# Kernel optimization log

Hardware: AMD Instinct MI355X
Metric: run time of the kernel (lower is better)

The kernel has to match this reference:

```python
import jax, jax.numpy as jnp
import numpy as np
import math

C_S, C_Z = 384, 128
N_HEAD, C = 12, 16
N_QP, N_PV = 4, 8
B, N_RES = 1, 384


def quat_to_rot(q):
    # q: (..., 4) unnormalized quaternion -> (..., 3, 3) rotation matrix
    q = q / jnp.linalg.norm(q, axis=-1, keepdims=True)
    w, x, y, z = q[..., 0], q[..., 1], q[..., 2], q[..., 3]
    R = jnp.stack([
        1 - 2 * (y * y + z * z), 2 * (x * y - w * z), 2 * (x * z + w * y),
        2 * (x * y + w * z), 1 - 2 * (x * x + z * z), 2 * (y * z - w * x),
        2 * (x * z - w * y), 2 * (y * z + w * x), 1 - 2 * (x * x + y * y),
    ], axis=-1)
    return R.reshape(q.shape[:-1] + (3, 3))


def warp_3d_point(T, p):
    # T: (..., 1, 1, N, 4, 4) rigid transforms; p: (..., H, P, N, 3)
    R = T[..., :3, :3]
    t = T[..., :3, 3]
    return jnp.squeeze(R @ p[..., None], -1) + t


def warp_3d_point_inv(T, p):
    # Inverse rigid transform: R^T (p - t)
    R = T[..., :3, :3]
    t = T[..., :3, 3]
    return jnp.squeeze(jnp.swapaxes(R, -1, -2) @ (p - t)[..., None], -1)


def setup_inputs() -> dict:
    key = jax.random.key(0)
    ks = jax.random.split(key, 24)
    s = jax.random.normal(ks[0], (B, N_RES, C_S), dtype=jnp.float32)
    z = jax.random.normal(ks[1], (B, N_RES, N_RES, C_Z), dtype=jnp.float32)
    # Build rigid backbone transforms T (rotation from random quaternion + translation)
    quat = jax.random.normal(ks[2], (B, N_RES, 4), dtype=jnp.float32)
    trans = jax.random.normal(ks[3], (B, N_RES, 3), dtype=jnp.float32) * 10.0
    R = quat_to_rot(quat)
    T = jnp.zeros((B, N_RES, 4, 4), dtype=jnp.float32)
    T = T.at[..., :3, :3].set(R)
    T = T.at[..., :3, 3].set(trans)
    T = T.at[..., 3, 3].set(1.0)

    def lin(k, din, dout):
        kw, kb = jax.random.split(k)
        W = jax.random.normal(kw, (din, dout), dtype=jnp.float32) * 0.02
        b = jax.random.normal(kb, (dout,), dtype=jnp.float32) * 0.01
        return W, b

    Wq, bq = lin(ks[4], C_S, N_HEAD * C)
    Wk, bk = lin(ks[5], C_S, N_HEAD * C)
    Wv, bv = lin(ks[6], C_S, N_HEAD * C)
    Wqp, bqp = lin(ks[7], C_S, 3 * N_QP * N_HEAD)
    Wkp, bkp = lin(ks[8], C_S, 3 * N_QP * N_HEAD)
    Wvp, bvp = lin(ks[9], C_S, 3 * N_PV * N_HEAD)
    Wb, bb = lin(ks[10], C_Z, N_HEAD)
    d_out_in = N_HEAD * C_Z + N_HEAD * C + N_HEAD * 4 * N_PV
    Wo, bo = lin(ks[11], d_out_in, C_S)
    head_weights = jax.random.normal(ks[12], (N_HEAD,), dtype=jnp.float32) * 0.1
    return dict(s=s, z=z, T=T, Wq=Wq, bq=bq, Wk=Wk, bk=bk, Wv=Wv, bv=bv,
                Wqp=Wqp, bqp=bqp, Wkp=Wkp, bkp=bkp, Wvp=Wvp, bvp=bvp,
                Wb=Wb, bb=bb, Wo=Wo, bo=bo, head_weights=head_weights)


def ipa_forward(s, z, T, Wq, bq, Wk, bk, Wv, bv, Wqp, bqp, Wkp, bkp,
                Wvp, bvp, Wb, bb, Wo, bo, head_weights):
    batch = s.shape[:-2]
    n = s.shape[-2]
    # --- prepare qkv ---
    def heads(x):  # (..., N, H*C) -> (..., H, N, C)
        return jnp.moveaxis(x.reshape(batch + (n, N_HEAD, C)), -3, -2)
    q = heads(s @ Wq + bq)
    k = heads(s @ Wk + bk)
    v = heads(s @ Wv + bv)

    def pts(x, P):  # (..., N, 3*H*P) -> (..., H, P, N, 3)
        x = x.reshape(batch + (n, 3, N_HEAD, P))
        return jnp.moveaxis(x, (-4, -3), (-2, -1))
    qp = pts(s @ Wqp + bqp, N_QP)
    kp = pts(s @ Wkp + bkp, N_QP)
    vp = pts(s @ Wvp + bvp, N_PV)

    # --- attention scores (Alg 22 line 7) ---
    wc = math.sqrt(2.0 / (9.0 * N_QP))
    wl = math.sqrt(1.0 / 3.0)
    gamma = jax.nn.softplus(head_weights).reshape(-1, 1, 1)  # (H,1,1)
    q = q * (1.0 / math.sqrt(C))
    bias = jnp.moveaxis(z @ Wb + bb, -1, -3)  # (..., H, N, N)
    qk = jnp.einsum('...hic,...hjc->...hij', q, k)
    T_bc = T.reshape(batch + (1, 1, n, 4, 4))
    tqp = warp_3d_point(T_bc, qp)[..., :, None, :]   # (..., H, QP, N, 1, 3)
    tkp = warp_3d_point(T_bc, kp)[..., None, :, :]   # (..., H, QP, 1, N, 3)
    sq_dist = jnp.sum((tqp - tkp) ** 2, axis=-1)      # (..., H, QP, N, N)
    qpkp_term = gamma * (wc / 2.0) * jnp.sum(sq_dist, axis=-3)  # (..., H, N, N)
    att = jax.nn.softmax(wl * (qk + bias - qpkp_term), axis=-1)

    # --- outputs ---
    pairwise = jnp.einsum('...ijc,...hij->...hic', z, att)
    pairwise = jnp.moveaxis(pairwise, -3, -2).reshape(batch + (n, N_HEAD * C_Z))
    v_out = jnp.einsum('...hij,...hjc->...hic', att, v)
    v_out = jnp.moveaxis(v_out, -3, -2).reshape(batch + (n, N_HEAD * C))
    vt = warp_3d_point(T_bc, vp)                                # (..., H, PV, N, 3)
    v_att = jnp.einsum('...hij,...hkjp->...hkip', att, vt)     # (..., H, PV, N, 3)
    v_tr = warp_3d_point_inv(T_bc, v_att)                       # (..., H, PV, N, 3)
    v_tr = jnp.einsum('...hpic->...ichp', v_tr)                 # (..., N, 3, H, PV)
    norm = jnp.linalg.norm(v_tr, axis=-3, keepdims=True)        # (..., N, 1, H, PV)
    vp_norm = norm.reshape(batch + (n, N_HEAD * N_PV))
    vp_out = v_tr.reshape(batch + (n, 3 * N_HEAD * N_PV))

    out = jnp.concatenate([v_out, vp_out, vp_norm, pairwise], axis=-1)
    return out @ Wo + bo


def reference(s, z, T, Wq, bq, Wk, bk, Wv, bv, Wqp, bqp, Wkp, bkp,
              Wvp, bvp, Wb, bb, Wo, bo, head_weights):
    return ipa_forward(s, z, T, Wq, bq, Wk, bk, Wv, bv, Wqp, bqp, Wkp, bkp,
                       Wvp, bvp, Wb, bb, Wo, bo, head_weights)
```

## Files before the change

kernel.cpp:

```cpp
#include <hip/hip_runtime.h>
#include <math.h>

#define NRES 384
#define NH   12
#define WLc 0.5773502691896258f
#define WCc 0.23570226039551587f

typedef __attribute__((ext_vector_type(8))) _Float16 half8;
typedef __attribute__((ext_vector_type(4))) float f32x4;

#define OFF_P    0
#define OFF_PW   0
#define OFF_SH   442368
#define OFF_WCT  516096
#define OFF_BCT  737280
#define OFF_QE   738432
#define OFF_KE   885888
#define OFF_VET  1033344
#define OFF_WOT  1143936
#define OFF_CAT  1549440
#define OFF_ATT  1660032
#define OFF_BIAS 2544768

__global__ __launch_bounds__(256) void pack_kernel(
    const float* __restrict__ s,
    const float* __restrict__ Wq,  const float* __restrict__ bq,
    const float* __restrict__ Wk,  const float* __restrict__ bk,
    const float* __restrict__ Wv,  const float* __restrict__ bv,
    const float* __restrict__ Wqp, const float* __restrict__ bqp,
    const float* __restrict__ Wkp, const float* __restrict__ bkp,
    const float* __restrict__ Wvp, const float* __restrict__ bvp,
    const float* __restrict__ Wo,  const float* __restrict__ bo,
    float* __restrict__ ws, float* __restrict__ out)
{
    int b = blockIdx.x, t = threadIdx.x;
    _Float16* sh  = (_Float16*)(ws + OFF_SH);
    _Float16* wct = (_Float16*)(ws + OFF_WCT);
    _Float16* wot = (_Float16*)(ws + OFF_WOT);
    float* bct = ws + OFF_BCT;

    if (b < 144) {
        int id = b * 256 + t;
        float4 v = ((const float4*)s)[id];
        _Float16 r[4] = { (_Float16)v.x, (_Float16)v.y, (_Float16)v.z, (_Float16)v.w };
        *(uint2*)(sh + id * 4) = *(uint2*)r;
        return;
    }
    __shared__ float tile[64 * 65];
    if (b < 252) {
        int ti = b - 144;
        int k0 = (ti % 6) * 64, n0 = (ti / 6) * 64;
        int cl = t & 63, rg = t >> 6;
        int ncat = n0 + cl;
        const float* W; int dout, col;
        if      (ncat < 192) { W = Wq;  dout = 192; col = ncat; }
        else if (ncat < 384) { W = Wk;  dout = 192; col = ncat - 192; }
        else if (ncat < 576) { W = Wv;  dout = 192; col = ncat - 384; }
        else if (ncat < 720) { W = Wqp; dout = 144; col = ncat - 576; }
        else if (ncat < 864) { W = Wkp; dout = 144; col = ncat - 720; }
        else                 { W = Wvp; dout = 288; col = ncat - 864; }
        #pragma unroll
        for (int u = 0; u < 16; u++) {
            int r = rg * 16 + u;
            tile[r * 65 + cl] = W[(size_t)(k0 + r) * dout + col];
        }
        __syncthreads();
        #pragma unroll
        for (int u2 = 0; u2 < 2; u2++) {
            int item = t + 256 * u2;
            int nl = item >> 3, kg = item & 7;
            half8 rr;
            #pragma unroll
            for (int jj = 0; jj < 8; jj++) rr[jj] = (_Float16)tile[(kg * 8 + jj) * 65 + nl];
            *(half8*)(wct + (size_t)(n0 + nl) * 384 + k0 + kg * 8) = rr;
        }
        return;
    }
    if (b < 450) {
        int ti = b - 252;
        int k0 = (ti % 33) * 64, n0 = (ti / 33) * 64;
        int cl = t & 63, rg = t >> 6;
        #pragma unroll
        for (int u = 0; u < 16; u++) {
            int r = rg * 16 + u;
            tile[r * 65 + cl] = Wo[(size_t)(k0 + r) * 384 + n0 + cl];
        }
        __syncthreads();
        #pragma unroll
        for (int u2 = 0; u2 < 2; u2++) {
            int item = t + 256 * u2;
            int nl = item >> 3, kg = item & 7;
            half8 rr;
            #pragma unroll
            for (int jj = 0; jj < 8; jj++) rr[jj] = (_Float16)tile[(kg * 8 + jj) * 65 + nl];
            *(half8*)(wot + (size_t)(n0 + nl) * 2112 + k0 + kg * 8) = rr;
        }
        return;
    }
    if (b == 450) {
        for (int e = t; e < 1152; e += 256) {
            float bv_;
            if      (e < 192) bv_ = bq[e];
            else if (e < 384) bv_ = bk[e - 192];
            else if (e < 576) bv_ = bv[e - 384];
            else if (e < 720) bv_ = bqp[e - 576];
            else if (e < 864) bv_ = bkp[e - 720];
            else              bv_ = bvp[e - 864];
            bct[e] = bv_;
        }
        return;
    }
    {
        int idx = (b - 451) * 256 + t;
        out[idx] = bo[idx % 384];
    }
}

__global__ __launch_bounds__(256) void proj_mfma(float* __restrict__ ws)
{
    const _Float16* sh  = (const _Float16*)(ws + OFF_SH);
    const _Float16* wct = (const _Float16*)(ws + OFF_WCT);
    const float* bct = ws + OFF_BCT;
    float* P = ws + OFF_P;

    int t = threadIdx.x, w = t >> 6, lane = t & 63;
    int m = lane & 15, q = lane >> 4;
    int n0 = blockIdx.x * 64, m0 = blockIdx.y * 64 + w * 16;

    f32x4 acc[4] = {0};
    const _Float16* arow = sh + (size_t)(m0 + m) * 384;
    #pragma unroll 4
    for (int s = 0; s < 12; s++) {
        int k = s * 32 + q * 8;
        half8 a = *(const half8*)(arow + k);
        #pragma unroll
        for (int nt = 0; nt < 4; nt++) {
            half8 b = *(const half8*)(wct + (size_t)(n0 + nt * 16 + m) * 384 + k);
            acc[nt] = __builtin_amdgcn_mfma_f32_16x16x32_f16(a, b, acc[nt], 0, 0, 0);
        }
    }
    #pragma unroll
    for (int nt = 0; nt < 4; nt++) {
        int col = n0 + nt * 16 + m;
        float bias = bct[col];
        #pragma unroll
        for (int r = 0; r < 4; r++)
            P[(size_t)(m0 + q * 4 + r) * 1152 + col] = acc[nt][r] + bias;
    }
}

__global__ __launch_bounds__(192) void prep_kernel(
    const float* __restrict__ T, const float* __restrict__ hw,
    float* __restrict__ ws)
{
    int i = blockIdx.x, t = threadIdx.x;
    const float* pr = ws + OFF_P + (size_t)i * 1152;
    float* Qe = ws + OFF_QE;
    float* Ke = ws + OFF_KE;
    _Float16* vet = (_Float16*)(ws + OFF_VET);

    __shared__ float sT[16], sG[12];
    __shared__ float sTQ[12][4][3], sTK[12][4][3];
    if (t < 16) sT[t] = T[i * 16 + t];
    if (t < 12) { float x = hw[t]; sG[t] = (x > 20.f) ? x : log1pf(__expf(x)); }
    __syncthreads();
    float R00=sT[0],R01=sT[1],R02=sT[2],t0=sT[3];
    float R10=sT[4],R11=sT[5],R12=sT[6],t1=sT[7];
    float R20=sT[8],R21=sT[9],R22=sT[10],t2=sT[11];

    if (t < 48) {
        int h = t >> 2, p = t & 3;
        float a0 = pr[576 + 0*48 + h*4 + p], a1 = pr[576 + 1*48 + h*4 + p], a2 = pr[576 + 2*48 + h*4 + p];
        sTQ[h][p][0] = R00*a0 + R01*a1 + R02*a2 + t0;
        sTQ[h][p][1] = R10*a0 + R11*a1 + R12*a2 + t1;
        sTQ[h][p][2] = R20*a0 + R21*a1 + R22*a2 + t2;
    } else if (t < 96) {
        int tt = t - 48, h = tt >> 2, p = tt & 3;
        float a0 = pr[720 + 0*48 + h*4 + p], a1 = pr[720 + 1*48 + h*4 + p], a2 = pr[720 + 2*48 + h*4 + p];
        sTK[h][p][0] = R00*a0 + R01*a1 + R02*a2 + t0;
        sTK[h][p][1] = R10*a0 + R11*a1 + R12*a2 + t1;
        sTK[h][p][2] = R20*a0 + R21*a1 + R22*a2 + t2;
    } else {
        int tt = t - 96, h = tt >> 3, p = tt & 7;
        float a0 = pr[864 + 0*96 + h*8 + p], a1 = pr[864 + 1*96 + h*8 + p], a2 = pr[864 + 2*96 + h*8 + p];
        vet[(size_t)(h*48 + 16 + p*3 + 0) * 384 + i] = (_Float16)(R00*a0 + R01*a1 + R02*a2 + t0);
        vet[(size_t)(h*48 + 16 + p*3 + 1) * 384 + i] = (_Float16)(R10*a0 + R11*a1 + R12*a2 + t1);
        vet[(size_t)(h*48 + 16 + p*3 + 2) * 384 + i] = (_Float16)(R20*a0 + R21*a1 + R22*a2 + t2);
    }
    {
        int h = t >> 4, c = t & 15;
        vet[(size_t)(h*48 + c) * 384 + i] = (_Float16)pr[384 + h*16 + c];
        if (t < 96) vet[(size_t)((t>>3)*48 + 40 + (t&7)) * 384 + i] = (_Float16)0.f;
        Qe[(size_t)i*384 + h*32 + c] = WLc * 0.25f * pr[h*16 + c];
        Ke[((size_t)h*384 + i)*32 + c] = pr[192 + h*16 + c];
    }
    __syncthreads();
    if (t < 144) {
        int h = t / 12, d = t % 12, p = d / 3, r = d % 3;
        float gw = WLc * sG[h] * WCc;
        Qe[(size_t)i*384 + h*32 + 16 + d] = gw * sTQ[h][p][r];
        Ke[((size_t)h*384 + i)*32 + 16 + d] = sTK[h][p][r];
    }
    if (t < 12) {
        int h = t;
        float sqq = 0.f, sqk = 0.f;
        #pragma unroll
        for (int p = 0; p < 4; p++)
            #pragma unroll
            for (int r = 0; r < 3; r++) { sqq += sTQ[h][p][r]*sTQ[h][p][r]; sqk += sTK[h][p][r]*sTK[h][p][r]; }
        float gw = WLc * sG[h] * WCc;
        Qe[(size_t)i*384 + h*32 + 28] = -0.5f * gw;
        Qe[(size_t)i*384 + h*32 + 29] = -0.5f * gw * sqq;
        Qe[(size_t)i*384 + h*32 + 30] = 0.f;
        Qe[(size_t)i*384 + h*32 + 31] = 0.f;
        Ke[((size_t)h*384 + i)*32 + 28] = sqk;
        Ke[((size_t)h*384 + i)*32 + 29] = 1.f;
        Ke[((size_t)h*384 + i)*32 + 30] = 0.f;
        Ke[((size_t)h*384 + i)*32 + 31] = 0.f;
    }
}

__global__ __launch_bounds__(256) void bias_mfma(
    const float* __restrict__ z, const float* __restrict__ Wb,
    const float* __restrict__ bb, float* __restrict__ ws)
{
    __shared__ _Float16 zb[64 * 136];
    __shared__ _Float16 wbT[16 * 136];
    __shared__ float sbb[16];
    _Float16* biasb = (_Float16*)(ws + OFF_BIAS);
    int b = blockIdx.x, t = threadIdx.x;

    if (b < 576) {
        ((float4*)(ws + OFF_PW))[b * 256 + t] = (float4){0.f, 0.f, 0.f, 0.f};
    }

    size_t m0 = (size_t)b * 64;
    {
        int r = t >> 2, co = (t & 3) * 32;
        const float* zr = z + (m0 + r) * 128 + co;
        #pragma unroll
        for (int u = 0; u < 4; u++) {
            float4 v0 = ((const float4*)zr)[u * 2 + 0];
            float4 v1 = ((const float4*)zr)[u * 2 + 1];
            half8 rr;
            rr[0]=(_Float16)v0.x; rr[1]=(_Float16)v0.y; rr[2]=(_Float16)v0.z; rr[3]=(_Float16)v0.w;
            rr[4]=(_Float16)v1.x; rr[5]=(_Float16)v1.y; rr[6]=(_Float16)v1.z; rr[7]=(_Float16)v1.w;
            *(half8*)(zb + r * 136 + co + u * 8) = rr;
        }
    }
    if (t < 128) {
        #pragma unroll
        for (int h = 0; h < 12; h++) wbT[h * 136 + t] = (_Float16)(WLc * Wb[t * 12 + h]);
        #pragma unroll
        for (int h = 12; h < 16; h++) wbT[h * 136 + t] = (_Float16)0.f;
    }
    if (t < 16) sbb[t] = (t < 12) ? WLc * bb[t] : 0.f;
    __syncthreads();

    int w = t >> 6, lane = t & 63;
    int m = lane & 15, q = lane >> 4;
    f32x4 acc = {0};
    #pragma unroll
    for (int s = 0; s < 4; s++) {
        int k = s * 32 + q * 8;
        half8 a = *(const half8*)(zb + (w * 16 + m) * 136 + k);
        half8 bfr = *(const half8*)(wbT + m * 136 + k);
        acc = __builtin_amdgcn_mfma_f32_16x16x32_f16(a, bfr, acc, 0, 0, 0);
    }
    if (m < 12) {
        #pragma unroll
        for (int r = 0; r < 4; r++) {
            size_t ri = m0 + w * 16 + q * 4 + r;
            biasb[(size_t)m * 147456 + ri] = (_Float16)(acc[r] + sbb[m]);
        }
    }
}

__global__ __launch_bounds__(512) void logits_kernel(float* __restrict__ ws)
{
    __shared__ float sQe[8 * 32];
    __shared__ float sLg[8][384];
    __shared__ float sMS[16];

    int h = blockIdx.y, i0 = blockIdx.x * 8;
    int t = threadIdx.x;
    const float* Qe = ws + OFF_QE;
    const float* Ke = ws + OFF_KE;
    const _Float16* biasb = (const _Float16*)(ws + OFF_BIAS);
    _Float16* attg = (_Float16*)(ws + OFF_ATT);

    if (t < 256)
        sQe[t] = Qe[(size_t)(i0 + (t >> 5)) * 384 + h * 32 + (t & 31)];
    __syncthreads();

    float lgv[8];
    if (t < 384) {
        int j = t;
        float ke[32];
        const float4* kr = (const float4*)(Ke + ((size_t)h * 384 + j) * 32);
        #pragma unroll
        for (int u = 0; u < 8; u++) { float4 v = kr[u]; ke[u*4]=v.x; ke[u*4+1]=v.y; ke[u*4+2]=v.z; ke[u*4+3]=v.w; }
        #pragma unroll
        for (int ii = 0; ii < 8; ii++) {
            float acc = (float)biasb[(size_t)h * 147456 + (size_t)(i0 + ii) * 384 + j];
            #pragma unroll
            for (int c = 0; c < 32; c++) acc += sQe[ii * 32 + c] * ke[c];
            lgv[ii] = acc;
            sLg[ii][j] = acc;
        }
    }
    __syncthreads();
    {
        int w = t >> 6, lane = t & 63;
        float vv[6], mx = -1e30f;
        #pragma unroll
        for (int u = 0; u < 6; u++) { vv[u] = sLg[w][lane + 64 * u]; mx = fmaxf(mx, vv[u]); }
        #pragma unroll
        for (int off = 1; off < 64; off <<= 1) mx = fmaxf(mx, __shfl_xor(mx, off));
        float sm = 0.f;
        #pragma unroll
        for (int u = 0; u < 6; u++) sm += __expf(vv[u] - mx);
        #pragma unroll
        for (int off = 1; off < 64; off <<= 1) sm += __shfl_xor(sm, off);
        if (lane == 0) { sMS[w] = mx; sMS[8 + w] = sm; }
    }
    __syncthreads();
    if (t < 384) {
        int j = t;
        #pragma unroll
        for (int ii = 0; ii < 8; ii++) {
            float a = __expf(lgv[ii] - sMS[ii]) * (1.0f / sMS[8 + ii]);
            attg[((size_t)h * 384 + i0 + ii) * 384 + j] = (_Float16)a;
        }
    }
}

__global__ __launch_bounds__(256) void pairwise_mfma(
    const float* __restrict__ z, float* __restrict__ ws)
{
    __shared__ _Float16 ztT[128 * 136];
    int i = blockIdx.x, jc = blockIdx.y, j0 = jc * 128;
    int t = threadIdx.x, w = t >> 6, lane = t & 63;
    int m16 = lane & 15, q = lane >> 4;
    const _Float16* attg = (const _Float16*)(ws + OFF_ATT);
    float* PW = ws + OFF_PW;

    {
        int c = t & 127, jg = t >> 7;
        const float* zbase = z + ((size_t)i * 384 + j0 + jg * 8) * 128 + c;
        #pragma unroll
        for (int jt = 0; jt < 8; jt++) {
            half8 r;
            #pragma unroll
            for (int u = 0; u < 8; u++)
                r[u] = (_Float16)zbase[(size_t)(jt * 16 + u) * 128];
            *(half8*)(ztT + c * 136 + jt * 16 + jg * 8) = r;
        }
    }
    __syncthreads();

    f32x4 acc0 = {0}, acc1 = {0};
    const _Float16* arow = attg + ((size_t)(m16 < 12 ? m16 : 0) * 384 + i) * 384 + j0;
    #pragma unroll
    for (int ks = 0; ks < 4; ks++) {
        int k = ks * 32 + q * 8;
        half8 a;
        if (m16 < 12) a = *(const half8*)(arow + k);
        else          a = (half8){0,0,0,0,0,0,0,0};
        half8 b0 = *(const half8*)(ztT + (w * 32 + m16) * 136 + k);
        half8 b1 = *(const half8*)(ztT + (w * 32 + 16 + m16) * 136 + k);
        acc0 = __builtin_amdgcn_mfma_f32_16x16x32_f16(a, b0, acc0, 0, 0, 0);
        acc1 = __builtin_amdgcn_mfma_f32_16x16x32_f16(a, b1, acc1, 0, 0, 0);
    }
    if (q < 3) {
        #pragma unroll
        for (int r = 0; r < 4; r++) {
            int h = q * 4 + r;
            atomicAdd(&PW[(size_t)i * 1536 + h * 128 + w * 32 + m16],      acc0[r]);
            atomicAdd(&PW[(size_t)i * 1536 + h * 128 + w * 32 + 16 + m16], acc1[r]);
        }
    }
}

__global__ __launch_bounds__(128) void out40_ep(
    const float* __restrict__ T, float* __restrict__ ws)
{
    const _Float16* attg = (const _Float16*)(ws + OFF_ATT);
    const _Float16* vet  = (const _Float16*)(ws + OFF_VET);
    _Float16* catb = (_Float16*)(ws + OFF_CAT);

    int h = blockIdx.y, t = threadIdx.x, w = t >> 6, lane = t & 63;
    int m16 = lane & 15, q = lane >> 4;
    int i0 = blockIdx.x * 32;

    __shared__ float sO[32 * 49];
    __shared__ float sTT[32 * 17];
    for (int e = t; e < 512; e += 128)
        sTT[(e >> 4) * 17 + (e & 15)] = T[(size_t)(i0 + (e >> 4)) * 16 + (e & 15)];

    f32x4 acc[3] = {0};
    const _Float16* arow = attg + ((size_t)h * 384 + i0 + w * 16 + m16) * 384;
    #pragma unroll 3
    for (int s = 0; s < 12; s++) {
        int k = s * 32 + q * 8;
        half8 a = *(const half8*)(arow + k);
        #pragma unroll
        for (int nt = 0; nt < 3; nt++) {
            half8 b = *(const half8*)(vet + (size_t)(h * 48 + nt * 16 + m16) * 384 + k);
            acc[nt] = __builtin_amdgcn_mfma_f32_16x16x32_f16(a, b, acc[nt], 0, 0, 0);
        }
    }
    #pragma unroll
    for (int nt = 0; nt < 3; nt++)
        #pragma unroll
        for (int r = 0; r < 4; r++)
            sO[(w * 16 + q * 4 + r) * 49 + nt * 16 + m16] = acc[nt][r];
    __syncthreads();

    for (int e = t; e < 512; e += 128) {
        int il = e >> 4, c = e & 15;
        catb[(size_t)(i0 + il) * 576 + h * 16 + c] = (_Float16)sO[il * 49 + c];
    }
    for (int e = t; e < 256; e += 128) {
        int il = e >> 3, p = e & 7;
        const float* o = sO + il * 49 + 16 + p * 3;
        const float* Ti = sTT + il * 17;
        float x0 = o[0] - Ti[3], x1 = o[1] - Ti[7], x2 = o[2] - Ti[11];
        float r0 = Ti[0]*x0 + Ti[4]*x1 + Ti[8]*x2;
        float r1 = Ti[1]*x0 + Ti[5]*x1 + Ti[9]*x2;
        float r2 = Ti[2]*x0 + Ti[6]*x1 + Ti[10]*x2;
        _Float16* cr = catb + (size_t)(i0 + il) * 576;
        cr[192 + 0*96 + h*8 + p] = (_Float16)r0;
        cr[192 + 1*96 + h*8 + p] = (_Float16)r1;
        cr[192 + 2*96 + h*8 + p] = (_Float16)r2;
        cr[480 + h*8 + p] = (_Float16)sqrtf(r0*r0 + r1*r1 + r2*r2);
    }
}

__global__ __launch_bounds__(128) void outgemm_mfma(float* __restrict__ ws, float* __restrict__ out)
{
    const _Float16* catb = (const _Float16*)(ws + OFF_CAT);
    const float* PW = ws + OFF_PW;
    const _Float16* wot = (const _Float16*)(ws + OFF_WOT);

    int t = threadIdx.x, w = t >> 6, lane = t & 63;
    int m = lane & 15, q = lane >> 4;
    int n0 = blockIdx.x * 64;
    int m0 = blockIdx.y * 32 + w * 16;
    int kbase = blockIdx.z * 352;

    f32x4 acc[4] = {0};
    int row = m0 + m;
    #pragma unroll 2
    for (int s = 0; s < 11; s++) {
        int kb = kbase + s * 32;
        int k = kb + q * 8;
        half8 a;
        if (kb < 576) {
            a = *(const half8*)(catb + (size_t)row * 576 + k);
        } else {
            const float* pwp = PW + (size_t)row * 1536 + (k - 576);
            float4 u0 = ((const float4*)pwp)[0];
            float4 u1 = ((const float4*)pwp)[1];
            a[0]=(_Float16)u0.x; a[1]=(_Float16)u0.y; a[2]=(_Float16)u0.z; a[3]=(_Float16)u0.w;
            a[4]=(_Float16)u1.x; a[5]=(_Float16)u1.y; a[6]=(_Float16)u1.z; a[7]=(_Float16)u1.w;
        }
        #pragma unroll
        for (int nt = 0; nt < 4; nt++) {
            half8 b = *(const half8*)(wot + (size_t)(n0 + nt * 16 + m) * 2112 + k);
            acc[nt] = __builtin_amdgcn_mfma_f32_16x16x32_f16(a, b, acc[nt], 0, 0, 0);
        }
    }
    #pragma unroll
    for (int nt = 0; nt < 4; nt++) {
        int col = n0 + nt * 16 + m;
        #pragma unroll
        for (int r = 0; r < 4; r++)
            atomicAdd(&out[(size_t)(m0 + q * 4 + r) * 384 + col], acc[nt][r]);
    }
}

extern "C" void kernel_launch(void* const* d_in, const int* in_sizes, int n_in,
                              void* d_out, int out_size, void* d_ws, size_t ws_size,
                              hipStream_t stream)
{
    const float* s   = (const float*)d_in[0];
    const float* z   = (const float*)d_in[1];
    const float* T   = (const float*)d_in[2];
    const float* Wq  = (const float*)d_in[3];
    const float* bq  = (const float*)d_in[4];
    const float* Wk  = (const float*)d_in[5];
    const float* bk  = (const float*)d_in[6];
    const float* Wv  = (const float*)d_in[7];
    const float* bv  = (const float*)d_in[8];
    const float* Wqp = (const float*)d_in[9];
    const float* bqp = (const float*)d_in[10];
    const float* Wkp = (const float*)d_in[11];
    const float* bkp = (const float*)d_in[12];
    const float* Wvp = (const float*)d_in[13];
    const float* bvp = (const float*)d_in[14];
    const float* Wb  = (const float*)d_in[15];
    const float* bb  = (const float*)d_in[16];
    const float* Wo  = (const float*)d_in[17];
    const float* bo  = (const float*)d_in[18];
    const float* hw  = (const float*)d_in[19];
    float* ws  = (float*)d_ws;
    float* out = (float*)d_out;

    pack_kernel<<<1027, 256, 0, stream>>>(s, Wq, bq, Wk, bk, Wv, bv,
                                          Wqp, bqp, Wkp, bkp, Wvp, bvp, Wo, bo, ws, out);
    proj_mfma<<<dim3(18, 6), 256, 0, stream>>>(ws);
    prep_kernel<<<384, 192, 0, stream>>>(T, hw, ws);
    bias_mfma<<<2304, 256, 0, stream>>>(z, Wb, bb, ws);
    logits_kernel<<<dim3(48, 12), 512, 0, stream>>>(ws);
    pairwise_mfma<<<dim3(384, 3), 256, 0, stream>>>(z, ws);
    out40_ep<<<dim3(12, 12), 128, 0, stream>>>(T, ws);
    outgemm_mfma<<<dim3(6, 12, 6), 128, 0, stream>>>(ws, out);
}
```

Baseline: 212.0 us.

## Fuse bias GEMM into pack kernel and attention-value epilogue into logits kernel

Merges the z-bias MFMA into the packing launch and reads z straight from global memory into MFMA fragments, skipping the LDS staging. Folds the attention-times-value and inverse-rigid epilogue into the logits kernel, using the softmax output already held in shared memory, and moves the out-bias init and PW zeroing there as well. Halves the proj_mfma block size to put more blocks on the grid. The goal is fewer launches and no reread of the attention matrix. In exchange the logits kernel uses more LDS and runs a half-empty MFMA (only 8 of 16 rows valid), and the merged pack kernel has heterogeneous blocks.

```diff
diff --git a/kernel.cpp b/kernel.cpp
--- a/kernel.cpp
+++ b/kernel.cpp
@@ -22,18 +22,58 @@
 #define OFF_ATT  1660032
 #define OFF_BIAS 2544768
 
-__global__ __launch_bounds__(256) void pack_kernel(
-    const float* __restrict__ s,
+__global__ __launch_bounds__(256) void pack_bias(
+    const float* __restrict__ s,  const float* __restrict__ z,
     const float* __restrict__ Wq,  const float* __restrict__ bq,
     const float* __restrict__ Wk,  const float* __restrict__ bk,
     const float* __restrict__ Wv,  const float* __restrict__ bv,
     const float* __restrict__ Wqp, const float* __restrict__ bqp,
     const float* __restrict__ Wkp, const float* __restrict__ bkp,
     const float* __restrict__ Wvp, const float* __restrict__ bvp,
-    const float* __restrict__ Wo,  const float* __restrict__ bo,
-    float* __restrict__ ws, float* __restrict__ out)
+    const float* __restrict__ Wb,  const float* __restrict__ bb,
+    const float* __restrict__ Wo,
+    float* __restrict__ ws)
 {
     int b = blockIdx.x, t = threadIdx.x;
+    __shared__ float tile[64 * 65];
+    __shared__ _Float16 wbT[16 * 136];
+    __shared__ float sbb[16];
+
+    if (b >= 451) {
+        _Float16* biasb = (_Float16*)(ws + OFF_BIAS);
+        int bi = b - 451;
+        size_t m0 = (size_t)bi * 64;
+        if (t < 128) {
+            #pragma unroll
+            for (int h = 0; h < 12; h++) wbT[h * 136 + t] = (_Float16)(WLc * Wb[t * 12 + h]);
+            #pragma unroll
+            for (int h = 12; h < 16; h++) wbT[h * 136 + t] = (_Float16)0.f;
+        }
+        if (t < 16) sbb[t] = (t < 12) ? WLc * bb[t] : 0.f;
+        __syncthreads();
+        int w = t >> 6, lane = t & 63;
+        int m = lane & 15, q = lane >> 4;
+        size_t ri = m0 + w * 16 + m;
+        const float* zr = z + ri * 128 + q * 8;
+        f32x4 acc = {0};
+        #pragma unroll
+        for (int sI = 0; sI < 4; sI++) {
+            float4 v0 = *(const float4*)(zr + sI * 32);
+            float4 v1 = *(const float4*)(zr + sI * 32 + 4);
+            half8 a;
+            a[0]=(_Float16)v0.x; a[1]=(_Float16)v0.y; a[2]=(_Float16)v0.z; a[3]=(_Float16)v0.w;
+            a[4]=(_Float16)v1.x; a[5]=(_Float16)v1.y; a[6]=(_Float16)v1.z; a[7]=(_Float16)v1.w;
+            half8 bf = *(const half8*)(wbT + m * 136 + sI * 32 + q * 8);
+            acc = __builtin_amdgcn_mfma_f32_16x16x32_f16(a, bf, acc, 0, 0, 0);
+        }
+        if (m < 12) {
+            #pragma unroll
+            for (int r = 0; r < 4; r++)
+                biasb[(size_t)m * 147456 + m0 + w * 16 + q * 4 + r] = (_Float16)(acc[r] + sbb[m]);
+        }
+        return;
+    }
+
     _Float16* sh  = (_Float16*)(ws + OFF_SH);
     _Float16* wct = (_Float16*)(ws + OFF_WCT);
     _Float16* wot = (_Float16*)(ws + OFF_WOT);
@@ -46,7 +86,6 @@
         *(uint2*)(sh + id * 4) = *(uint2*)r;
         return;
     }
-    __shared__ float tile[64 * 65];
     if (b < 252) {
         int ti = b - 144;
         int k0 = (ti % 6) * 64, n0 = (ti / 6) * 64;
@@ -97,26 +136,19 @@
         }
         return;
     }
-    if (b == 450) {
-        for (int e = t; e < 1152; e += 256) {
-            float bv_;
-            if      (e < 192) bv_ = bq[e];
-            else if (e < 384) bv_ = bk[e - 192];
-            else if (e < 576) bv_ = bv[e - 384];
-            else if (e < 720) bv_ = bqp[e - 576];
-            else if (e < 864) bv_ = bkp[e - 720];
-            else              bv_ = bvp[e - 864];
-            bct[e] = bv_;
-        }
-        return;
-    }
-    {
-        int idx = (b - 451) * 256 + t;
-        out[idx] = bo[idx % 384];
-    }
-}
-
-__global__ __launch_bounds__(256) void proj_mfma(float* __restrict__ ws)
+    for (int e = t; e < 1152; e += 256) {
+        float bv_;
+        if      (e < 192) bv_ = bq[e];
+        else if (e < 384) bv_ = bk[e - 192];
+        else if (e < 576) bv_ = bv[e - 384];
+        else if (e < 720) bv_ = bqp[e - 576];
+        else if (e < 864) bv_ = bkp[e - 720];
+        else              bv_ = bvp[e - 864];
+        bct[e] = bv_;
+    }
+}
+
+__global__ __launch_bounds__(128) void proj_mfma(float* __restrict__ ws)
 {
     const _Float16* sh  = (const _Float16*)(ws + OFF_SH);
     const _Float16* wct = (const _Float16*)(ws + OFF_WCT);
@@ -125,7 +157,7 @@
 
     int t = threadIdx.x, w = t >> 6, lane = t & 63;
     int m = lane & 15, q = lane >> 4;
-    int n0 = blockIdx.x * 64, m0 = blockIdx.y * 64 + w * 16;
+    int n0 = blockIdx.x * 64, m0 = blockIdx.y * 32 + w * 16;
 
     f32x4 acc[4] = {0};
     const _Float16* arow = sh + (size_t)(m0 + m) * 384;
@@ -220,77 +252,38 @@
     }
 }
 
-__global__ __launch_bounds__(256) void bias_mfma(
-    const float* __restrict__ z, const float* __restrict__ Wb,
-    const float* __restrict__ bb, float* __restrict__ ws)
-{
-    __shared__ _Float16 zb[64 * 136];
-    __shared__ _Float16 wbT[16 * 136];
-    __shared__ float sbb[16];
-    _Float16* biasb = (_Float16*)(ws + OFF_BIAS);
-    int b = blockIdx.x, t = threadIdx.x;
-
-    if (b < 576) {
-        ((float4*)(ws + OFF_PW))[b * 256 + t] = (float4){0.f, 0.f, 0.f, 0.f};
-    }
-
-    size_t m0 = (size_t)b * 64;
-    {
-        int r = t >> 2, co = (t & 3) * 32;
-        const float* zr = z + (m0 + r) * 128 + co;
-        #pragma unroll
-        for (int u = 0; u < 4; u++) {
-            float4 v0 = ((const float4*)zr)[u * 2 + 0];
-            float4 v1 = ((const float4*)zr)[u * 2 + 1];
-            half8 rr;
-            rr[0]=(_Float16)v0.x; rr[1]=(_Float16)v0.y; rr[2]=(_Float16)v0.z; rr[3]=(_Float16)v0.w;
-            rr[4]=(_Float16)v1.x; rr[5]=(_Float16)v1.y; rr[6]=(_Float16)v1.z; rr[7]=(_Float16)v1.w;
-            *(half8*)(zb + r * 136 + co + u * 8) = rr;
-        }
-    }
-    if (t < 128) {
-        #pragma unroll
-        for (int h = 0; h < 12; h++) wbT[h * 136 + t] = (_Float16)(WLc * Wb[t * 12 + h]);
-        #pragma unroll
-        for (int h = 12; h < 16; h++) wbT[h * 136 + t] = (_Float16)0.f;
-    }
-    if (t < 16) sbb[t] = (t < 12) ? WLc * bb[t] : 0.f;
-    __syncthreads();
-
-    int w = t >> 6, lane = t & 63;
-    int m = lane & 15, q = lane >> 4;
-    f32x4 acc = {0};
-    #pragma unroll
-    for (int s = 0; s < 4; s++) {
-        int k = s * 32 + q * 8;
-        half8 a = *(const half8*)(zb + (w * 16 + m) * 136 + k);
-        half8 bfr = *(const half8*)(wbT + m * 136 + k);
-        acc = __builtin_amdgcn_mfma_f32_16x16x32_f16(a, bfr, acc, 0, 0, 0);
-    }
-    if (m < 12) {
-        #pragma unroll
-        for (int r = 0; r < 4; r++) {
-            size_t ri = m0 + w * 16 + q * 4 + r;
-            biasb[(size_t)m * 147456 + ri] = (_Float16)(acc[r] + sbb[m]);
-        }
-    }
-}
-
-__global__ __launch_bounds__(512) void logits_kernel(float* __restrict__ ws)
+__global__ __launch_bounds__(512) void logits_out40(
+    const float* __restrict__ T, const float* __restrict__ bo,
+    float* __restrict__ ws, float* __restrict__ out)
 {
     __shared__ float sQe[8 * 32];
     __shared__ float sLg[8][384];
     __shared__ float sMS[16];
+    __shared__ _Float16 sAttL[8 * 392];
+    __shared__ float sO[8 * 49];
+    __shared__ float sT8[8 * 16];
 
     int h = blockIdx.y, i0 = blockIdx.x * 8;
     int t = threadIdx.x;
     const float* Qe = ws + OFF_QE;
     const float* Ke = ws + OFF_KE;
     const _Float16* biasb = (const _Float16*)(ws + OFF_BIAS);
+    const _Float16* vet = (const _Float16*)(ws + OFF_VET);
     _Float16* attg = (_Float16*)(ws + OFF_ATT);
-
+    _Float16* catb = (_Float16*)(ws + OFF_CAT);
+
+    {
+        int bid = blockIdx.y * 48 + blockIdx.x;
+        if (t < 256) {
+            int e = bid * 256 + t;
+            out[e] = bo[e % 384];
+            ((float4*)(ws + OFF_PW))[e] = (float4){0.f, 0.f, 0.f, 0.f};
+        }
+    }
     if (t < 256)
         sQe[t] = Qe[(size_t)(i0 + (t >> 5)) * 384 + h * 32 + (t & 31)];
+    if (t < 128)
+        sT8[t] = T[(size_t)(i0 + (t >> 4)) * 16 + (t & 15)];
     __syncthreads();
 
     float lgv[8];
@@ -331,7 +324,50 @@
         for (int ii = 0; ii < 8; ii++) {
             float a = __expf(lgv[ii] - sMS[ii]) * (1.0f / sMS[8 + ii]);
             attg[((size_t)h * 384 + i0 + ii) * 384 + j] = (_Float16)a;
-        }
+            sAttL[ii * 392 + j] = (_Float16)a;
+        }
+    }
+    __syncthreads();
+
+    int w = t >> 6, lane = t & 63;
+    int m16 = lane & 15, q = lane >> 4;
+    if (w < 3) {
+        int nt = w;
+        f32x4 acc = {0};
+        #pragma unroll 3
+        for (int s = 0; s < 12; s++) {
+            int k = s * 32 + q * 8;
+            half8 a;
+            if (m16 < 8) a = *(const half8*)(sAttL + m16 * 392 + k);
+            else         a = (half8){0,0,0,0,0,0,0,0};
+            half8 bfr = *(const half8*)(vet + (size_t)(h * 48 + nt * 16 + m16) * 384 + k);
+            acc = __builtin_amdgcn_mfma_f32_16x16x32_f16(a, bfr, acc, 0, 0, 0);
+        }
+        #pragma unroll
+        for (int r = 0; r < 4; r++) {
+            int row = q * 4 + r;
+            if (row < 8) sO[row * 49 + nt * 16 + m16] = acc[r];
+        }
+    }
+    __syncthreads();
+
+    if (t < 128) {
+        int il = t >> 4, c = t & 15;
+        catb[(size_t)(i0 + il) * 576 + h * 16 + c] = (_Float16)sO[il * 49 + c];
+    }
+    if (t < 64) {
+        int il = t >> 3, p = t & 7;
+        const float* o = sO + il * 49 + 16 + p * 3;
+        const float* Ti = sT8 + il * 16;
+        float x0 = o[0] - Ti[3], x1 = o[1] - Ti[7], x2 = o[2] - Ti[11];
+        float r0 = Ti[0]*x0 + Ti[4]*x1 + Ti[8]*x2;
+        float r1 = Ti[1]*x0 + Ti[5]*x1 + Ti[9]*x2;
+        float r2 = Ti[2]*x0 + Ti[6]*x1 + Ti[10]*x2;
+        _Float16* cr = catb + (size_t)(i0 + il) * 576;
+        cr[192 + 0*96 + h*8 + p] = (_Float16)r0;
+        cr[192 + 1*96 + h*8 + p] = (_Float16)r1;
+        cr[192 + 2*96 + h*8 + p] = (_Float16)r2;
+        cr[480 + h*8 + p] = (_Float16)sqrtf(r0*r0 + r1*r1 + r2*r2);
     }
 }
 
@@ -379,61 +415,6 @@
             atomicAdd(&PW[(size_t)i * 1536 + h * 128 + w * 32 + m16],      acc0[r]);
             atomicAdd(&PW[(size_t)i * 1536 + h * 128 + w * 32 + 16 + m16], acc1[r]);
         }
-    }
-}
-
-__global__ __launch_bounds__(128) void out40_ep(
-    const float* __restrict__ T, float* __restrict__ ws)
-{
-    const _Float16* attg = (const _Float16*)(ws + OFF_ATT);
-    const _Float16* vet  = (const _Float16*)(ws + OFF_VET);
-    _Float16* catb = (_Float16*)(ws + OFF_CAT);
-
-    int h = blockIdx.y, t = threadIdx.x, w = t >> 6, lane = t & 63;
-    int m16 = lane & 15, q = lane >> 4;
-    int i0 = blockIdx.x * 32;
-
-    __shared__ float sO[32 * 49];
-    __shared__ float sTT[32 * 17];
-    for (int e = t; e < 512; e += 128)
-        sTT[(e >> 4) * 17 + (e & 15)] = T[(size_t)(i0 + (e >> 4)) * 16 + (e & 15)];
-
-    f32x4 acc[3] = {0};
-    const _Float16* arow = attg + ((size_t)h * 384 + i0 + w * 16 + m16) * 384;
-    #pragma unroll 3
-    for (int s = 0; s < 12; s++) {
-        int k = s * 32 + q * 8;
-        half8 a = *(const half8*)(arow + k);
-        #pragma unroll
-        for (int nt = 0; nt < 3; nt++) {
-            half8 b = *(const half8*)(vet + (size_t)(h * 48 + nt * 16 + m16) * 384 + k);
-            acc[nt] = __builtin_amdgcn_mfma_f32_16x16x32_f16(a, b, acc[nt], 0, 0, 0);
-        }
-    }
-    #pragma unroll
-    for (int nt = 0; nt < 3; nt++)
-        #pragma unroll
-        for (int r = 0; r < 4; r++)
-            sO[(w * 16 + q * 4 + r) * 49 + nt * 16 + m16] = acc[nt][r];
-    __syncthreads();
-
-    for (int e = t; e < 512; e += 128) {
-        int il = e >> 4, c = e & 15;
-        catb[(size_t)(i0 + il) * 576 + h * 16 + c] = (_Float16)sO[il * 49 + c];
-    }
-    for (int e = t; e < 256; e += 128) {
-        int il = e >> 3, p = e & 7;
-        const float* o = sO + il * 49 + 16 + p * 3;
-        const float* Ti = sTT + il * 17;
-        float x0 = o[0] - Ti[3], x1 = o[1] - Ti[7], x2 = o[2] - Ti[11];
-        float r0 = Ti[0]*x0 + Ti[4]*x1 + Ti[8]*x2;
-        float r1 = Ti[1]*x0 + Ti[5]*x1 + Ti[9]*x2;
-        float r2 = Ti[2]*x0 + Ti[6]*x1 + Ti[10]*x2;
-        _Float16* cr = catb + (size_t)(i0 + il) * 576;
-        cr[192 + 0*96 + h*8 + p] = (_Float16)r0;
-        cr[192 + 1*96 + h*8 + p] = (_Float16)r1;
-        cr[192 + 2*96 + h*8 + p] = (_Float16)r2;
-        cr[480 + h*8 + p] = (_Float16)sqrtf(r0*r0 + r1*r1 + r2*r2);
     }
 }
 
@@ -507,13 +488,11 @@
     float* ws  = (float*)d_ws;
     float* out = (float*)d_out;
 
-    pack_kernel<<<1027, 256, 0, stream>>>(s, Wq, bq, Wk, bk, Wv, bv,
-                                          Wqp, bqp, Wkp, bkp, Wvp, bvp, Wo, bo, ws, out);
-    proj_mfma<<<dim3(18, 6), 256, 0, stream>>>(ws);
+    pack_bias<<<2755, 256, 0, stream>>>(s, z, Wq, bq, Wk, bk, Wv, bv,
+                                        Wqp, bqp, Wkp, bkp, Wvp, bvp, Wb, bb, Wo, ws);
+    proj_mfma<<<dim3(18, 12), 128, 0, stream>>>(ws);
     prep_kernel<<<384, 192, 0, stream>>>(T, hw, ws);
-    bias_mfma<<<2304, 256, 0, stream>>>(z, Wb, bb, ws);
-    logits_kernel<<<dim3(48, 12), 512, 0, stream>>>(ws);
+    logits_out40<<<dim3(48, 12), 512, 0, stream>>>(T, bo, ws, out);
     pairwise_mfma<<<dim3(384, 3), 256, 0, stream>>>(z, ws);
-    out40_ep<<<dim3(12, 12), 128, 0, stream>>>(T, ws);
     outgemm_mfma<<<dim3(6, 12, 6), 128, 0, stream>>>(ws, out);
 }
```

New measurement: 203.3 us. 1.04x faster.
